# Performance work log

Measured on AMD Instinct MI355X. Metric: run time of the kernel, lower is better.

## Reference

```python
import jax, jax.numpy as jnp
import numpy as np

EMBED_DIM = 1024
NUM_HEADS = 16
HEAD_DIM = EMBED_DIM // NUM_HEADS
SCALE = HEAD_DIM ** -0.5


def setup_inputs() -> dict:
    key = jax.random.key(0)
    k_x, k_wqkv, k_bqkv, k_wp, k_bp = jax.random.split(key, 5)
    B, N = 2, 2048
    x = jax.random.normal(k_x, (B, N, EMBED_DIM), dtype=jnp.float32)
    # torch.nn.Linear default init: U(-1/sqrt(fan_in), 1/sqrt(fan_in))
    lim = 1.0 / np.sqrt(EMBED_DIM)
    W_qkv = jax.random.uniform(k_wqkv, (EMBED_DIM, 3 * EMBED_DIM), jnp.float32, -lim, lim)
    b_qkv = jax.random.uniform(k_bqkv, (3 * EMBED_DIM,), jnp.float32, -lim, lim)
    W_proj = jax.random.uniform(k_wp, (EMBED_DIM, EMBED_DIM), jnp.float32, -lim, lim)
    b_proj = jax.random.uniform(k_bp, (EMBED_DIM,), jnp.float32, -lim, lim)
    return {"x": x, "W_qkv": W_qkv, "b_qkv": b_qkv, "W_proj": W_proj, "b_proj": b_proj}


def reference(x, W_qkv, b_qkv, W_proj, b_proj):
    B, N, C = x.shape
    qkv = x @ W_qkv + b_qkv                              # [B, N, 3C]
    qkv = qkv.reshape(B, N, 3, NUM_HEADS, HEAD_DIM)
    qkv = jnp.transpose(qkv, (2, 0, 3, 1, 4))            # [3, B, H, N, D]
    q, k, v = qkv[0], qkv[1], qkv[2]
    attn = jnp.einsum('bhnd,bhmd->bhnm', q, k) * SCALE   # [B, H, N, N]
    attn = jax.nn.softmax(attn, axis=-1)
    out = jnp.einsum('bhnm,bhmd->bhnd', attn, v)         # [B, H, N, D]
    out = jnp.transpose(out, (0, 2, 1, 3)).reshape(B, N, C)
    return out @ W_proj + b_proj
```

## Files before the change

### kernel.cpp

```cpp
#include <hip/hip_runtime.h>
#include <math.h>

typedef unsigned short u16;
typedef _Float16 f16;
typedef f16 f16x8 __attribute__((ext_vector_type(8)));
typedef __fp16 hp16x2 __attribute__((ext_vector_type(2)));
typedef float f32x4 __attribute__((ext_vector_type(4)));
typedef float f32x16 __attribute__((ext_vector_type(16)));
typedef unsigned u32x2 __attribute__((ext_vector_type(2)));

#define SEQ   2048
#define NH    16
#define HD    64
#define EMB   1024
#define NQKV  3072
#define BATCH 2
#define QSCALE 0.18033688f

__device__ __forceinline__ u16 f2h(float f) {
  union { f16 h; u16 u; } w; w.h = (f16)f; return w.u;
}

__device__ __forceinline__ void gload16(const void* g, void* l) {
  __builtin_amdgcn_global_load_lds(
      (const __attribute__((address_space(1))) unsigned int*)g,
      (__attribute__((address_space(3))) unsigned int*)l, 16, 0, 0);
}

__device__ __forceinline__ void cvt_wt_tile(const float* __restrict__ W,
                                            u16* __restrict__ Wt,
                                            int K, int N, int n0, int k0, int t) {
  __shared__ u16 T[64][68];
  const int rr = t >> 4, cc = (t & 15) << 2;
#pragma unroll
  for (int p = 0; p < 4; p++) {
    const int kr = p * 16 + rr;
    float4 v = *reinterpret_cast<const float4*>(&W[(size_t)(k0 + kr) * N + n0 + cc]);
    T[cc + 0][kr] = f2h(v.x); T[cc + 1][kr] = f2h(v.y);
    T[cc + 2][kr] = f2h(v.z); T[cc + 3][kr] = f2h(v.w);
  }
  __syncthreads();
#pragma unroll
  for (int p = 0; p < 4; p++) {
    const int nr = p * 16 + rr;
    union { u16 s[4]; unsigned long long d; } o;
    o.s[0] = T[nr][cc + 0]; o.s[1] = T[nr][cc + 1];
    o.s[2] = T[nr][cc + 2]; o.s[3] = T[nr][cc + 3];
    *reinterpret_cast<unsigned long long*>(&Wt[(size_t)(n0 + nr) * K + k0 + cc]) = o.d;
  }
}

__global__ __launch_bounds__(256) void k_pre(const float* __restrict__ X,
                                             u16* __restrict__ Xh,
                                             const float* __restrict__ Wqkv,
                                             u16* __restrict__ Wt,
                                             const float* __restrict__ Wproj,
                                             u16* __restrict__ Wpt) {
  const int b = blockIdx.x;
  const int t = threadIdx.x;
  if (b < 2048) {
    const size_t i = ((size_t)b * 256 + t) * 8;
    float4 a = *reinterpret_cast<const float4*>(&X[i]);
    float4 c = *reinterpret_cast<const float4*>(&X[i + 4]);
    union { hp16x2 h2[4]; float4 f; } pk;
    pk.h2[0] = __builtin_amdgcn_cvt_pkrtz(a.x, a.y);
    pk.h2[1] = __builtin_amdgcn_cvt_pkrtz(a.z, a.w);
    pk.h2[2] = __builtin_amdgcn_cvt_pkrtz(c.x, c.y);
    pk.h2[3] = __builtin_amdgcn_cvt_pkrtz(c.z, c.w);
    *reinterpret_cast<float4*>(&Xh[i]) = pk.f;
  } else if (b < 2048 + 768) {
    const int id = b - 2048;
    cvt_wt_tile(Wqkv, Wt, EMB, NQKV, (id % 48) << 6, (id / 48) << 6, t);
  } else {
    const int id = b - 2816;
    cvt_wt_tile(Wproj, Wpt, EMB, EMB, (id % 16) << 6, (id / 16) << 6, t);
  }
}

__device__ __forceinline__ void gemm_core(const u16* __restrict__ Ag,
                                          const u16* __restrict__ Bg,
                                          int m0, int n0, int t,
                                          f32x4 acc[4][4]) {
  __shared__ __align__(16) u16 As[2][128 * 32];
  __shared__ __align__(16) u16 Bs[2][128 * 32];
  const int lane = t & 63, w = t >> 6;
  const int l15  = lane & 15, quad = lane >> 4;
  const int wm = w >> 1, wn = w & 1;
  const int srow  = lane >> 2;
  const int gslot = (lane & 3) ^ ((srow >> 1) & 3);
  const int xk    = (quad ^ ((l15 >> 1) & 3)) << 3;

  auto STAGE = [&](int buf, int k0) {
#pragma unroll
    for (int i = 0; i < 2; i++) {
      const int ca = w * 2 + i;
      const int arow = ca * 16 + srow;
      gload16(Ag + (size_t)(m0 + arow) * EMB + k0 + gslot * 8, &As[buf][ca * 512]);
      gload16(Bg + (size_t)(n0 + arow) * EMB + k0 + gslot * 8, &Bs[buf][ca * 512]);
    }
  };

  STAGE(0, 0);
  __syncthreads();

  for (int kt = 0; kt < EMB / 32; ++kt) {
    if (kt + 1 < EMB / 32) STAGE((kt + 1) & 1, (kt + 1) * 32);
    const u16* Asb = As[kt & 1];
    const u16* Bsb = Bs[kt & 1];
    f16x8 af[4], bf[4];
#pragma unroll
    for (int s = 0; s < 4; s++)
      af[s] = *reinterpret_cast<const f16x8*>(&Asb[(wm * 64 + s * 16 + l15) * 32 + xk]);
#pragma unroll
    for (int s = 0; s < 4; s++)
      bf[s] = *reinterpret_cast<const f16x8*>(&Bsb[(wn * 64 + s * 16 + l15) * 32 + xk]);
    __builtin_amdgcn_s_setprio(1);
#pragma unroll
    for (int i = 0; i < 4; i++)
#pragma unroll
      for (int j = 0; j < 4; j++)
        acc[i][j] = __builtin_amdgcn_mfma_f32_16x16x32_f16(af[i], bf[j], acc[i][j], 0, 0, 0);
    __builtin_amdgcn_s_setprio(0);
    __syncthreads();
  }
}

__device__ __forceinline__ void gemm_core_sb(const u16* __restrict__ Ag,
                                             const u16* __restrict__ Bg,
                                             int m0, int n0, int t,
                                             f32x4 acc[4][4]) {
  __shared__ __align__(16) u16 As[128 * 32];
  __shared__ __align__(16) u16 Bs[128 * 32];
  const int lane = t & 63, w = t >> 6;
  const int l15  = lane & 15, quad = lane >> 4;
  const int wm = w >> 1, wn = w & 1;
  const int srow  = lane >> 2;
  const int gslot = (lane & 3) ^ ((srow >> 1) & 3);
  const int xk    = (quad ^ ((l15 >> 1) & 3)) << 3;

  for (int k0 = 0; k0 < EMB; k0 += 32) {
    __syncthreads();
#pragma unroll
    for (int i = 0; i < 2; i++) {
      const int ca = w * 2 + i;
      const int arow = ca * 16 + srow;
      gload16(Ag + (size_t)(m0 + arow) * EMB + k0 + gslot * 8, &As[ca * 512]);
      gload16(Bg + (size_t)(n0 + arow) * EMB + k0 + gslot * 8, &Bs[ca * 512]);
    }
    __syncthreads();
    f16x8 af[4], bf[4];
#pragma unroll
    for (int s = 0; s < 4; s++)
      af[s] = *reinterpret_cast<const f16x8*>(&As[(wm * 64 + s * 16 + l15) * 32 + xk]);
#pragma unroll
    for (int s = 0; s < 4; s++)
      bf[s] = *reinterpret_cast<const f16x8*>(&Bs[(wn * 64 + s * 16 + l15) * 32 + xk]);
#pragma unroll
    for (int i = 0; i < 4; i++)
#pragma unroll
      for (int j = 0; j < 4; j++)
        acc[i][j] = __builtin_amdgcn_mfma_f32_16x16x32_f16(af[i], bf[j], acc[i][j], 0, 0, 0);
  }
}

__global__ __launch_bounds__(256) void k_qkv(const u16* __restrict__ Ag,
                                             const u16* __restrict__ Bg,
                                             const float* __restrict__ bias,
                                             u16* __restrict__ qo,
                                             u16* __restrict__ ko,
                                             u16* __restrict__ vo) {
  const int t = threadIdx.x;
  const int lane = t & 63, w = t >> 6;
  const int l15 = lane & 15, quad = lane >> 4;
  const int wm = w >> 1, wn = w & 1;
  const int id  = blockIdx.y * 24 + blockIdx.x;
  const int xcd = id & 7, r = id >> 3;
  const int n_t = 12 * (xcd & 1) + r % 12;
  const int m_t = 8 * (xcd >> 1) + r / 12;
  const int m0 = m_t << 7, n0 = n_t << 7;
  f32x4 acc[4][4];
#pragma unroll
  for (int i = 0; i < 4; i++)
#pragma unroll
    for (int j = 0; j < 4; j++) acc[i][j] = (f32x4){0.f, 0.f, 0.f, 0.f};
  gemm_core(Ag, Bg, m0, n0, t, acc);
#pragma unroll
  for (int j = 0; j < 4; j++) {
    const int c = n0 + wn * 64 + j * 16 + l15;
    const int which = c >> 10, h = (c >> 6) & 15, d = c & 63;
    const float bv = bias[c];
    const float sc = (which == 0) ? QSCALE : 1.0f;
#pragma unroll
    for (int i = 0; i < 4; i++) {
#pragma unroll
      for (int r2 = 0; r2 < 4; r2++) {
        const int m  = m0 + wm * 64 + i * 16 + quad * 4 + r2;
        const int bb = m >> 11, n = m & (SEQ - 1);
        const u16 val = f2h((acc[i][j][r2] + bv) * sc);
        if (which == 2)
          vo[(((size_t)bb * NH + h) * HD + d) * SEQ + n] = val;
        else if (which == 1)
          ko[((((size_t)bb * NH + h) * SEQ) + n) * HD + d] = val;
        else
          qo[((((size_t)bb * NH + h) * SEQ) + n) * HD + d] = val;
      }
    }
  }
}

__global__ __launch_bounds__(256) void k_proj(const u16* __restrict__ Ag,
                                              const u16* __restrict__ Bg,
                                              const float* __restrict__ bias,
                                              float* __restrict__ out) {
  const int t = threadIdx.x;
  const int lane = t & 63, w = t >> 6;
  const int l15 = lane & 15, quad = lane >> 4;
  const int wm = w >> 1, wn = w & 1;
  const int m0 = blockIdx.y << 7, n0 = blockIdx.x << 7;
  f32x4 acc[4][4];
#pragma unroll
  for (int i = 0; i < 4; i++)
#pragma unroll
    for (int j = 0; j < 4; j++) acc[i][j] = (f32x4){0.f, 0.f, 0.f, 0.f};
  gemm_core_sb(Ag, Bg, m0, n0, t, acc);
#pragma unroll
  for (int j = 0; j < 4; j++) {
    const int c = n0 + wn * 64 + j * 16 + l15;
    const float bv = bias[c];
#pragma unroll
    for (int i = 0; i < 4; i++) {
#pragma unroll
      for (int r2 = 0; r2 < 4; r2++) {
        const int m = m0 + wm * 64 + i * 16 + quad * 4 + r2;
        out[(size_t)m * EMB + c] = acc[i][j][r2] + bv;
      }
    }
  }
}

__global__ __launch_bounds__(512, 4) void k_attn(const u16* __restrict__ Qg,
                                                 const u16* __restrict__ Kg,
                                                 const u16* __restrict__ Vtg,
                                                 u16* __restrict__ AO) {
  __shared__ __align__(16) u16 KV[2][2][2][64 * 64];
  __shared__ float Lx[256];
  const int t    = threadIdx.x;
  const int lane = t & 63, w = t >> 6;
  const int grp  = w >> 2, wl = w & 3;
  const int l31  = lane & 31, hi = lane >> 5;
  const int id   = blockIdx.y * 16 + blockIdx.x;
  const int swz  = ((id & 7) << 6) | (id >> 3);
  const int bh   = swz >> 4;
  const int q0   = (swz & 15) << 7;
  const size_t base = (size_t)bh * SEQ * HD;

  f16x8 qf[4];
  {
    const u16* qp = Qg + base + (size_t)(q0 + 32 * wl + l31) * HD + hi * 8;
#pragma unroll
    for (int c = 0; c < 4; c++) {
      union { float4 f; f16x8 v; } fu;
      fu.f = *reinterpret_cast<const float4*>(qp + c * 16);
      qf[c] = fu.v;
    }
  }

  f32x16 O0 = {}, O1 = {};
  float lsum = 0.f;
  const int fsw = (l31 >> 1) & 7;
  const int srw = lane >> 3, ssl = lane & 7;
  const int kbeg = grp << 10;
  const int kend = kbeg + (SEQ / 2);

  auto STAGE = [&](int buf, int kt) {
    u16* Ksb = KV[buf][grp][0];
    u16* Vsb = KV[buf][grp][1];
#pragma unroll
    for (int i = 0; i < 2; i++) {
      const int ca  = wl * 2 + i;
      const int row = ca * 8 + srw;
      const int sg  = (ssl ^ ((row >> 1) & 7)) << 3;
      gload16(Kg  + base + (size_t)(kt + row) * HD + sg, &Ksb[ca * 512]);
      gload16(Vtg + base + (size_t)row * SEQ + kt + sg,  &Vsb[ca * 512]);
    }
  };

  STAGE(0, kbeg);
  __syncthreads();

  int cur = 0;
  for (int kt = kbeg; kt < kend; kt += 64) {
    if (kt + 64 < kend) STAGE(cur ^ 1, kt + 64);
    const u16* Ks = KV[cur][grp][0];
    const u16* Vs = KV[cur][grp][1];

#pragma unroll
    for (int sk = 0; sk < 2; sk++) {
      f32x16 c = {};
      __builtin_amdgcn_s_setprio(1);
#pragma unroll
      for (int cc = 0; cc < 4; cc++) {
        f16x8 kf = *reinterpret_cast<const f16x8*>(
            &Ks[(sk * 32 + l31) * 64 + (((cc * 2 + hi) ^ fsw) << 3)]);
        c = __builtin_amdgcn_mfma_f32_32x32x16_f16(kf, qf[cc], c, 0, 0, 0);
      }
      __builtin_amdgcn_s_setprio(0);
      unsigned pw[4][2];
#pragma unroll
      for (int g = 0; g < 4; g++) {
        const float p0 = __builtin_amdgcn_exp2f(c[4 * g + 0]);
        const float p1 = __builtin_amdgcn_exp2f(c[4 * g + 1]);
        const float p2 = __builtin_amdgcn_exp2f(c[4 * g + 2]);
        const float p3 = __builtin_amdgcn_exp2f(c[4 * g + 3]);
        lsum += (p0 + p1) + (p2 + p3);
        union { hp16x2 h; unsigned u; } w0, w1;
        w0.h = __builtin_amdgcn_cvt_pkrtz(p0, p1);
        w1.h = __builtin_amdgcn_cvt_pkrtz(p2, p3);
        pw[g][0] = w0.u; pw[g][1] = w1.u;
      }
      __builtin_amdgcn_s_setprio(1);
#pragma unroll
      for (int s = 0; s < 2; s++) {
        u32x2 r02 = __builtin_amdgcn_permlane32_swap(
            pw[2 * s][0], pw[2 * s + 1][0], false, false);
        u32x2 r13 = __builtin_amdgcn_permlane32_swap(
            pw[2 * s][1], pw[2 * s + 1][1], false, false);
        union { unsigned u[4]; f16x8 v; } fr;
        fr.u[0] = r02.x;
        fr.u[1] = r13.x;
        fr.u[2] = r02.y;
        fr.u[3] = r13.y;
        const int cc = sk * 2 + s;
        f16x8 vf0 = *reinterpret_cast<const f16x8*>(
            &Vs[l31 * 64 + (((cc * 2 + hi) ^ fsw) << 3)]);
        f16x8 vf1 = *reinterpret_cast<const f16x8*>(
            &Vs[(32 + l31) * 64 + (((cc * 2 + hi) ^ fsw) << 3)]);
        O0 = __builtin_amdgcn_mfma_f32_32x32x16_f16(fr.v, vf0, O0, 0, 0, 0);
        O1 = __builtin_amdgcn_mfma_f32_32x32x16_f16(fr.v, vf1, O1, 0, 0, 0);
      }
      __builtin_amdgcn_s_setprio(0);
    }
    __syncthreads();
    cur ^= 1;
  }

  float* Xch = reinterpret_cast<float*>(&KV[0][0][0][0]);
  const int li = wl * 64 + lane;
  if (grp == 1) {
#pragma unroll
    for (int g4 = 0; g4 < 4; g4++) {
      f32x4 v0 = { O0[4 * g4 + 0], O0[4 * g4 + 1], O0[4 * g4 + 2], O0[4 * g4 + 3] };
      *reinterpret_cast<f32x4*>(&Xch[(g4 * 256 + li) * 4]) = v0;
      f32x4 v1 = { O1[4 * g4 + 0], O1[4 * g4 + 1], O1[4 * g4 + 2], O1[4 * g4 + 3] };
      *reinterpret_cast<f32x4*>(&Xch[((4 + g4) * 256 + li) * 4]) = v1;
    }
    Lx[li] = lsum;
  }
  __syncthreads();
  if (grp == 0) {
#pragma unroll
    for (int g4 = 0; g4 < 4; g4++) {
      f32x4 v0 = *reinterpret_cast<const f32x4*>(&Xch[(g4 * 256 + li) * 4]);
      f32x4 v1 = *reinterpret_cast<const f32x4*>(&Xch[((4 + g4) * 256 + li) * 4]);
#pragma unroll
      for (int j = 0; j < 4; j++) {
        O0[4 * g4 + j] += v0[j];
        O1[4 * g4 + j] += v1[j];
      }
    }
    lsum += Lx[li];
    lsum += __shfl_xor(lsum, 32);
    const int b = bh >> 4, h = bh & 15;
#pragma unroll
    for (int g = 0; g < 4; g++) {
#pragma unroll
      for (int rr = 0; rr < 4; rr++) {
        const int r = g * 4 + rr;
        const int qrow = rr + 8 * g + 4 * hi;
        const float inv = 1.f / __shfl(lsum, qrow, 64);
        const int n = q0 + 32 * wl + qrow;
        u16* dst = AO + ((size_t)(b * SEQ + n)) * EMB + h * HD;
        dst[l31]      = f2h(O0[r] * inv);
        dst[32 + l31] = f2h(O1[r] * inv);
      }
    }
  }
}

extern "C" void kernel_launch(void* const* d_in, const int* in_sizes, int n_in,
                              void* d_out, int out_size, void* d_ws, size_t ws_size,
                              hipStream_t stream) {
  (void)in_sizes; (void)n_in; (void)out_size; (void)ws_size;
  const float* x     = (const float*)d_in[0];
  const float* Wqkv  = (const float*)d_in[1];
  const float* bqkv  = (const float*)d_in[2];
  const float* Wproj = (const float*)d_in[3];
  const float* bproj = (const float*)d_in[4];
  float* out = (float*)d_out;

  const size_t NE = (size_t)BATCH * SEQ * EMB;
  u16* q    = (u16*)d_ws;
  u16* k    = q + NE;
  u16* vt   = k + NE;
  u16* aoxh = vt + NE;
  u16* Wt   = aoxh + NE;
  u16* Wpt  = Wt + (size_t)NQKV * EMB;

  k_pre<<<3072, 256, 0, stream>>>(x, aoxh, Wqkv, Wt, Wproj, Wpt);

  dim3 gq(NQKV / 128, (BATCH * SEQ) / 128);
  k_qkv<<<gq, 256, 0, stream>>>(aoxh, Wt, bqkv, q, k, vt);

  dim3 ga(SEQ / 128, BATCH * NH);
  k_attn<<<ga, 512, 0, stream>>>(q, k, vt, aoxh);

  dim3 gp(EMB / 128, (BATCH * SEQ) / 128);
  k_proj<<<gp, 256, 0, stream>>>(aoxh, Wpt, bproj, out);
}
```

Baseline: 193.5 us.

## Restructure QKV GEMM to 8 waves with BK=64 double-buffered swizzled tiles

The QKV projection kernel gets its own inlined GEMM loop. It now uses 512 threads (8 waves, arranged 2x4), each computing a 64x32 sub-tile, and the K step grows from 32 to 64 with an 8-slot XOR swizzle in LDS. This halves the number of K iterations and barriers and puts more waves on each tile to hide latency. In exchange it doubles LDS use per block (64 KB double-buffered) and lowers MFMA reuse per wave, which may limit occupancy.

```diff
diff --git a/kernel.cpp b/kernel.cpp
--- a/kernel.cpp
+++ b/kernel.cpp
@@ -77,54 +77,6 @@
   }
 }
 
-__device__ __forceinline__ void gemm_core(const u16* __restrict__ Ag,
-                                          const u16* __restrict__ Bg,
-                                          int m0, int n0, int t,
-                                          f32x4 acc[4][4]) {
-  __shared__ __align__(16) u16 As[2][128 * 32];
-  __shared__ __align__(16) u16 Bs[2][128 * 32];
-  const int lane = t & 63, w = t >> 6;
-  const int l15  = lane & 15, quad = lane >> 4;
-  const int wm = w >> 1, wn = w & 1;
-  const int srow  = lane >> 2;
-  const int gslot = (lane & 3) ^ ((srow >> 1) & 3);
-  const int xk    = (quad ^ ((l15 >> 1) & 3)) << 3;
-
-  auto STAGE = [&](int buf, int k0) {
-#pragma unroll
-    for (int i = 0; i < 2; i++) {
-      const int ca = w * 2 + i;
-      const int arow = ca * 16 + srow;
-      gload16(Ag + (size_t)(m0 + arow) * EMB + k0 + gslot * 8, &As[buf][ca * 512]);
-      gload16(Bg + (size_t)(n0 + arow) * EMB + k0 + gslot * 8, &Bs[buf][ca * 512]);
-    }
-  };
-
-  STAGE(0, 0);
-  __syncthreads();
-
-  for (int kt = 0; kt < EMB / 32; ++kt) {
-    if (kt + 1 < EMB / 32) STAGE((kt + 1) & 1, (kt + 1) * 32);
-    const u16* Asb = As[kt & 1];
-    const u16* Bsb = Bs[kt & 1];
-    f16x8 af[4], bf[4];
-#pragma unroll
-    for (int s = 0; s < 4; s++)
-      af[s] = *reinterpret_cast<const f16x8*>(&Asb[(wm * 64 + s * 16 + l15) * 32 + xk]);
-#pragma unroll
-    for (int s = 0; s < 4; s++)
-      bf[s] = *reinterpret_cast<const f16x8*>(&Bsb[(wn * 64 + s * 16 + l15) * 32 + xk]);
-    __builtin_amdgcn_s_setprio(1);
-#pragma unroll
-    for (int i = 0; i < 4; i++)
-#pragma unroll
-      for (int j = 0; j < 4; j++)
-        acc[i][j] = __builtin_amdgcn_mfma_f32_16x16x32_f16(af[i], bf[j], acc[i][j], 0, 0, 0);
-    __builtin_amdgcn_s_setprio(0);
-    __syncthreads();
-  }
-}
-
 __device__ __forceinline__ void gemm_core_sb(const u16* __restrict__ Ag,
                                              const u16* __restrict__ Bg,
                                              int m0, int n0, int t,
@@ -163,30 +115,77 @@
   }
 }
 
-__global__ __launch_bounds__(256) void k_qkv(const u16* __restrict__ Ag,
-                                             const u16* __restrict__ Bg,
-                                             const float* __restrict__ bias,
-                                             u16* __restrict__ qo,
-                                             u16* __restrict__ ko,
-                                             u16* __restrict__ vo) {
+__global__ __launch_bounds__(512, 4) void k_qkv(const u16* __restrict__ Ag,
+                                                const u16* __restrict__ Bg,
+                                                const float* __restrict__ bias,
+                                                u16* __restrict__ qo,
+                                                u16* __restrict__ ko,
+                                                u16* __restrict__ vo) {
+  __shared__ __align__(16) u16 As[2][128 * 64];
+  __shared__ __align__(16) u16 Bs[2][128 * 64];
   const int t = threadIdx.x;
   const int lane = t & 63, w = t >> 6;
   const int l15 = lane & 15, quad = lane >> 4;
-  const int wm = w >> 1, wn = w & 1;
+  const int wm = w >> 2, wn = w & 3;
+  const int srw = lane >> 3, ssl = lane & 7;
+  const int fsw = (l15 >> 1) & 7;
   const int id  = blockIdx.y * 24 + blockIdx.x;
-  const int xcd = id & 7, r = id >> 3;
-  const int n_t = 12 * (xcd & 1) + r % 12;
-  const int m_t = 8 * (xcd >> 1) + r / 12;
+  const int xcd = id & 7, rr = id >> 3;
+  const int n_t = 12 * (xcd & 1) + rr % 12;
+  const int m_t = 8 * (xcd >> 1) + rr / 12;
   const int m0 = m_t << 7, n0 = n_t << 7;
-  f32x4 acc[4][4];
+
+  f32x4 acc[4][2];
 #pragma unroll
   for (int i = 0; i < 4; i++)
 #pragma unroll
-    for (int j = 0; j < 4; j++) acc[i][j] = (f32x4){0.f, 0.f, 0.f, 0.f};
-  gemm_core(Ag, Bg, m0, n0, t, acc);
-#pragma unroll
-  for (int j = 0; j < 4; j++) {
-    const int c = n0 + wn * 64 + j * 16 + l15;
+    for (int j = 0; j < 2; j++) acc[i][j] = (f32x4){0.f, 0.f, 0.f, 0.f};
+
+  auto STAGE = [&](int buf, int k0) {
+#pragma unroll
+    for (int i = 0; i < 2; i++) {
+      const int ca  = w * 2 + i;
+      const int row = ca * 8 + srw;
+      const int sg  = (ssl ^ ((row >> 1) & 7)) << 3;
+      gload16(Ag + (size_t)(m0 + row) * EMB + k0 + sg, &As[buf][ca * 512]);
+      gload16(Bg + (size_t)(n0 + row) * EMB + k0 + sg, &Bs[buf][ca * 512]);
+    }
+  };
+
+  STAGE(0, 0);
+  __syncthreads();
+
+  for (int kt = 0; kt < 16; ++kt) {
+    if (kt + 1 < 16) STAGE((kt + 1) & 1, (kt + 1) * 64);
+    const u16* Asb = As[kt & 1];
+    const u16* Bsb = Bs[kt & 1];
+#pragma unroll
+    for (int ks = 0; ks < 2; ks++) {
+      const int gsl = ((ks * 4 + quad) ^ fsw) << 3;
+      f16x8 af[4], bf[2];
+#pragma unroll
+      for (int s = 0; s < 4; s++)
+        af[s] = *reinterpret_cast<const f16x8*>(
+            &Asb[(wm * 64 + s * 16 + l15) * 64 + gsl]);
+#pragma unroll
+      for (int s = 0; s < 2; s++)
+        bf[s] = *reinterpret_cast<const f16x8*>(
+            &Bsb[(wn * 32 + s * 16 + l15) * 64 + gsl]);
+      __builtin_amdgcn_s_setprio(1);
+#pragma unroll
+      for (int i = 0; i < 4; i++)
+#pragma unroll
+        for (int j = 0; j < 2; j++)
+          acc[i][j] = __builtin_amdgcn_mfma_f32_16x16x32_f16(af[i], bf[j],
+                                                             acc[i][j], 0, 0, 0);
+      __builtin_amdgcn_s_setprio(0);
+    }
+    __syncthreads();
+  }
+
+#pragma unroll
+  for (int j = 0; j < 2; j++) {
+    const int c = n0 + wn * 32 + j * 16 + l15;
     const int which = c >> 10, h = (c >> 6) & 15, d = c & 63;
     const float bv = bias[c];
     const float sc = (which == 0) ? QSCALE : 1.0f;
@@ -409,7 +408,7 @@
   k_pre<<<3072, 256, 0, stream>>>(x, aoxh, Wqkv, Wt, Wproj, Wpt);
 
   dim3 gq(NQKV / 128, (BATCH * SEQ) / 128);
-  k_qkv<<<gq, 256, 0, stream>>>(aoxh, Wt, bqkv, q, k, vt);
+  k_qkv<<<gq, 512, 0, stream>>>(aoxh, Wt, bqkv, q, k, vt);
 
   dim3 ga(SEQ / 128, BATCH * NH);
   k_attn<<<ga, 512, 0, stream>>>(q, k, vt, aoxh);
```

Result: no change. 196.0 us (+1.3%).
